# Performance work log

Hardware: AMD Instinct MI355X
Metric: run time of the kernel (lower is better)

Reference implementation:

```python
import jax, jax.numpy as jnp
import numpy as np

B, S, T = 512, 512, 128


def setup_inputs() -> dict:
    key = jax.random.key(0)
    k1, k2, k3, k4, k5 = jax.random.split(key, 5)
    emissions = jax.random.normal(k1, (B, S, T), dtype=jnp.float32)
    tags = jax.random.randint(k2, (B, S), 0, T, dtype=jnp.int32)
    mask = jnp.ones((B, S), dtype=jnp.int32)
    start_transitions = jax.random.uniform(k3, (T,), minval=-0.1, maxval=0.1, dtype=jnp.float32)
    end_transitions = jax.random.uniform(k4, (T,), minval=-0.1, maxval=0.1, dtype=jnp.float32)
    transitions = jax.random.uniform(k5, (T, T), minval=-0.1, maxval=0.1, dtype=jnp.float32)
    return {"emissions": emissions, "tags": tags, "mask": mask,
            "start_transitions": start_transitions,
            "end_transitions": end_transitions,
            "transitions": transitions}


def reference(emissions, tags, mask, start_transitions, end_transitions, transitions):
    b, s, t = emissions.shape
    maskf = mask.astype(emissions.dtype)
    barange = jnp.arange(b)

    # ---- numerator: score of the gold path (vectorized over timesteps) ----
    score = start_transitions[tags[:, 0]] + emissions[barange, 0, tags[:, 0]]
    # transition scores tags[i-1] -> tags[i], shape (B, S-1)
    trans_steps = transitions[tags[:, :-1], tags[:, 1:]]
    # emission score of gold tag at each step, shape (B, S)
    em_steps = jnp.take_along_axis(emissions, tags[:, :, None], axis=2)[:, :, 0]
    score = score + jnp.sum((trans_steps + em_steps[:, 1:]) * maskf[:, 1:], axis=1)
    seq_ends = mask.astype(jnp.int32).sum(axis=1) - 1
    last_tags = tags[barange, seq_ends]
    score = score + end_transitions[last_tags]

    # ---- denominator: log partition via forward recurrence (lax.scan) ----
    init = start_transitions[None, :] + emissions[:, 0, :]  # (B, T)

    def step(scores, inp):
        em_i, m_i = inp  # (B, T), (B,)
        # (B, T_prev, T_next) semiring matmul in log-space
        nxt = jax.nn.logsumexp(
            scores[:, :, None] + transitions[None, :, :] + em_i[:, None, :], axis=1)
        scores = jnp.where(m_i[:, None] > 0, nxt, scores)
        return scores, None

    ems = jnp.moveaxis(emissions[:, 1:, :], 1, 0)  # (S-1, B, T)
    ms = jnp.moveaxis(mask[:, 1:], 1, 0)           # (S-1, B)
    final, _ = jax.lax.scan(step, init, (ems, ms))
    denom = jax.nn.logsumexp(final + end_transitions[None, :], axis=1)  # (B,)

    return jnp.sum(score - denom)
```

## Files before the change

### kernel.cpp

```cpp
#include <hip/hip_runtime.h>
#include <math.h>


#define T 128
#define SLEN 512
#define BATCH 512

typedef float v2f __attribute__((ext_vector_type(2)));

static __device__ __forceinline__ float dpp_xor1(float x) {
    return __int_as_float(__builtin_amdgcn_update_dpp(
        0, __float_as_int(x), 0xB1, 0xF, 0xF, true));
}
static __device__ __forceinline__ float dpp_xor2(float x) {
    return __int_as_float(__builtin_amdgcn_update_dpp(
        0, __float_as_int(x), 0x4E, 0xF, 0xF, true));
}
static __device__ __forceinline__ void lgkm_barrier() {
    asm volatile("s_waitcnt lgkmcnt(0)\n\ts_barrier" ::: "memory");
}
static __device__ __forceinline__ int pslot(int j) {
    return j ^ (((j >> 5) & 3) << 2);
}

__global__ __launch_bounds__(512, 4) void fwd_kernel(
    const float* __restrict__ em, const int* __restrict__ tags,
    const int* __restrict__ mask, const float* __restrict__ startT,
    const float* __restrict__ endT, const float* __restrict__ trans,
    float* __restrict__ ws)
{
    const int tid  = threadIdx.x;
    const int lane = tid & 63;
    const int w    = tid >> 6;
    const int rg   = lane & 3;
    const int cg   = lane >> 2;
    const int b    = blockIdx.x;
    const int mycol = 16 * w + cg;

    const float* emb = em + (size_t)b * SLEN * T;
    const int*   mk  = mask + (size_t)b * SLEN;

    __shared__ __align__(16) float p_lds[2][T];
    __shared__ float reds[8], redn[8];
    __shared__ int   redc[8];

    int rslot[8];
#pragma unroll
    for (int k = 0; k < 8; ++k)
        rslot[k] = (32 * rg + 4 * k) ^ (rg << 2);
    const int wslot = pslot(mycol);

    v2f Elo[8], Ehi[8];
#pragma unroll
    for (int k = 0; k < 8; ++k) {
        const float* tp = trans + (32 * rg + 4 * k) * T + mycol;
        Elo[k] = (v2f){ __expf(tp[0 * T]), __expf(tp[1 * T]) };
        Ehi[k] = (v2f){ __expf(tp[2 * T]), __expf(tp[3 * T]) };
    }

    float pprev = __expf(startT[mycol] + emb[mycol]);
    if (rg == 0) p_lds[1][wslot] = pprev;
    double Ld = 0.0;

    float emv[4], emn[4];
    int   mkv[4], mkn[4];
#pragma unroll
    for (int k = 0; k < 4; ++k) {
        emv[k] = __expf(emb[(1 + k) * T + mycol]);
        mkv[k] = mk[1 + k];
    }
    lgkm_barrier();

    for (int s0 = 1; s0 < SLEN; s0 += 4) {
#pragma unroll
        for (int k = 0; k < 4; ++k) {
            int ss = s0 + 4 + k; ss = (ss < SLEN) ? ss : (SLEN - 1);
            emn[k] = emb[ss * T + mycol];
            mkn[k] = mk[ss];
        }
#pragma unroll
        for (int k = 0; k < 4; ++k) {
            const int s = s0 + k;
            if (s < SLEN) {
                const int cur = (1 + k) & 1;
                const float srefc = fmaxf(p_lds[cur][0], 1e-30f);
                const float cc = __builtin_amdgcn_rcpf(srefc);
                Ld += (double)__logf(srefc);

                v2f pk0[8], pk1[8];
#pragma unroll
                for (int k2 = 0; k2 < 8; ++k2) {
                    const float4 pv = *(const float4*)&p_lds[cur][rslot[k2]];
                    pk0[k2] = (v2f){ pv.x, pv.y };
                    pk1[k2] = (v2f){ pv.z, pv.w };
                }
                v2f accE = pk0[0] * Elo[0];
                v2f accO = pk1[0] * Ehi[0];
#pragma unroll
                for (int k2 = 1; k2 < 8; ++k2) {
                    accE = __builtin_elementwise_fma(pk0[k2], Elo[k2], accE);
                    accO = __builtin_elementwise_fma(pk1[k2], Ehi[k2], accO);
                }
                const v2f accT = accE + accO;
                const float sv = accT.x + accT.y;

                float t = sv + dpp_xor1(sv);
                t = t + dpp_xor2(t);

                const float pn = t * (emv[k] * cc);
                const float pm = pprev * cc;
                pprev = (mkv[k] > 0) ? pn : pm;
                if (rg == 0) p_lds[cur ^ 1][wslot] = pprev;
                lgkm_barrier();
            }
        }
#pragma unroll
        for (int k = 0; k < 4; ++k) { emv[k] = __expf(emn[k]); mkv[k] = mkn[k]; }
    }

    const float eendv = __expf(endT[mycol]);
    float sm = pprev * eendv;
#pragma unroll
    for (int off = 32; off; off >>= 1) sm += __shfl_xor(sm, off);
    if (lane == 0) reds[w] = sm;

    const int* tg = tags + (size_t)b * SLEN;
    float nv = 0.f; int cnt = 0;
    {
        const int s = tid;
        const int mm = mk[s];
        cnt += (mm != 0);
        if (s >= 1 && mm > 0)
            nv += trans[tg[s - 1] * T + tg[s]] + emb[s * T + tg[s]];
    }
#pragma unroll
    for (int off = 32; off; off >>= 1) {
        nv  += __shfl_xor(nv, off);
        cnt += __shfl_xor(cnt, off);
    }
    if (lane == 0) { redn[w] = nv; redc[w] = cnt; }
    __syncthreads();
    if (tid == 0) {
        float ssum = 0.f, nsum = 0.f; int seqlen = 0;
#pragma unroll
        for (int i = 0; i < 8; ++i) {
            ssum += reds[i]; nsum += redn[i]; seqlen += redc[i];
        }
        const float denom = __logf(0.25f * ssum) + (float)Ld;
        const int t0g = tg[0], tl = tg[seqlen - 1];
        ws[b] = (startT[t0g] + emb[t0g] + endT[tl] + nsum) - denom;
    }
}

__global__ __launch_bounds__(256) void reduce_kernel(
    const float* __restrict__ ws, float* __restrict__ out)
{
    const int t = threadIdx.x;
    float local = 0.f;
    for (int i = t; i < BATCH; i += 256) local += ws[i];
    __shared__ float rf[256];
    rf[t] = local;
    __syncthreads();
    for (int off = 128; off > 0; off >>= 1) {
        if (t < off) rf[t] += rf[t + off];
        __syncthreads();
    }
    if (t == 0) out[0] = rf[0];
}

extern "C" void kernel_launch(void* const* d_in, const int* in_sizes, int n_in,
                              void* d_out, int out_size, void* d_ws, size_t ws_size,
                              hipStream_t stream)
{
    const float* emissions = (const float*)d_in[0];
    const int*   tags      = (const int*)d_in[1];
    const int*   mask      = (const int*)d_in[2];
    const float* startT    = (const float*)d_in[3];
    const float* endT      = (const float*)d_in[4];
    const float* trans     = (const float*)d_in[5];
    float* out = (float*)d_out;
    float* ws  = (float*)d_ws;

    fwd_kernel<<<BATCH, 512, 0, stream>>>(emissions, tags, mask, startT, endT, trans, ws);
    reduce_kernel<<<1, 256, 0, stream>>>(ws, out);
}
```

Before: 392.2 us.

## Halve block size with two columns per lane and renormalize once per four steps

Each thread now computes two output columns of the forward recurrence, so a block needs 256 threads instead of 512, and the transition matrix held in registers doubles. The rescaling by the reference probability and the log accumulation now happen only on the first of every four timesteps rather than every step, which removes an LDS read, a reciprocal and a double-precision add from most steps. The per-step DPP reduction is restructured so that the two partial sums per lane pair combine into the right column. Skipping renormalization on three of four steps risks float overflow or underflow over those steps, and the extra registers may lower occupancy.

```diff
diff --git a/kernel.cpp b/kernel.cpp
--- a/kernel.cpp
+++ b/kernel.cpp
@@ -23,7 +23,7 @@
     return j ^ (((j >> 5) & 3) << 2);
 }
 
-__global__ __launch_bounds__(512, 4) void fwd_kernel(
+__global__ __launch_bounds__(256, 2) void fwd_kernel(
     const float* __restrict__ em, const int* __restrict__ tags,
     const int* __restrict__ mask, const float* __restrict__ startT,
     const float* __restrict__ endT, const float* __restrict__ trans,
@@ -35,31 +35,36 @@
     const int rg   = lane & 3;
     const int cg   = lane >> 2;
     const int b    = blockIdx.x;
-    const int mycol = 16 * w + cg;
+    const int rb0  = rg & 1;
+    const int colbase = 32 * w + 2 * cg;
+    const int mycol   = colbase + rb0;
 
     const float* emb = em + (size_t)b * SLEN * T;
     const int*   mk  = mask + (size_t)b * SLEN;
 
     __shared__ __align__(16) float p_lds[2][T];
-    __shared__ float reds[8], redn[8];
-    __shared__ int   redc[8];
+    __shared__ float reds[4], redn[4];
+    __shared__ int   redc[4];
 
     int rslot[8];
 #pragma unroll
-    for (int k = 0; k < 8; ++k)
-        rslot[k] = (32 * rg + 4 * k) ^ (rg << 2);
+    for (int k2 = 0; k2 < 8; ++k2)
+        rslot[k2] = 32 * rg + 4 * (k2 ^ rg);
     const int wslot = pslot(mycol);
 
-    v2f Elo[8], Ehi[8];
-#pragma unroll
-    for (int k = 0; k < 8; ++k) {
-        const float* tp = trans + (32 * rg + 4 * k) * T + mycol;
-        Elo[k] = (v2f){ __expf(tp[0 * T]), __expf(tp[1 * T]) };
-        Ehi[k] = (v2f){ __expf(tp[2 * T]), __expf(tp[3 * T]) };
+    v2f Elo[2][8], Ehi[2][8];
+#pragma unroll
+    for (int k2 = 0; k2 < 8; ++k2) {
+        const float* tp = trans + (32 * rg + 4 * k2) * T + colbase;
+#pragma unroll
+        for (int c = 0; c < 2; ++c) {
+            Elo[c][k2] = (v2f){ __expf(tp[0 * T + c]), __expf(tp[1 * T + c]) };
+            Ehi[c][k2] = (v2f){ __expf(tp[2 * T + c]), __expf(tp[3 * T + c]) };
+        }
     }
 
     float pprev = __expf(startT[mycol] + emb[mycol]);
-    if (rg == 0) p_lds[1][wslot] = pprev;
+    if (rg < 2) p_lds[1][wslot] = pprev;
     double Ld = 0.0;
 
     float emv[4], emn[4];
@@ -83,9 +88,12 @@
             const int s = s0 + k;
             if (s < SLEN) {
                 const int cur = (1 + k) & 1;
-                const float srefc = fmaxf(p_lds[cur][0], 1e-30f);
-                const float cc = __builtin_amdgcn_rcpf(srefc);
-                Ld += (double)__logf(srefc);
+                float cc = 1.0f;
+                if (k == 0) {
+                    const float srefc = fmaxf(p_lds[cur][0], 1e-30f);
+                    cc = __builtin_amdgcn_rcpf(srefc);
+                    Ld += (double)__logf(srefc);
+                }
 
                 v2f pk0[8], pk1[8];
 #pragma unroll
@@ -94,23 +102,30 @@
                     pk0[k2] = (v2f){ pv.x, pv.y };
                     pk1[k2] = (v2f){ pv.z, pv.w };
                 }
-                v2f accE = pk0[0] * Elo[0];
-                v2f accO = pk1[0] * Ehi[0];
+                v2f a0e = pk0[0] * Elo[0][0];
+                v2f a0o = pk1[0] * Ehi[0][0];
+                v2f a1e = pk0[0] * Elo[1][0];
+                v2f a1o = pk1[0] * Ehi[1][0];
 #pragma unroll
                 for (int k2 = 1; k2 < 8; ++k2) {
-                    accE = __builtin_elementwise_fma(pk0[k2], Elo[k2], accE);
-                    accO = __builtin_elementwise_fma(pk1[k2], Ehi[k2], accO);
+                    a0e = __builtin_elementwise_fma(pk0[k2], Elo[0][k2], a0e);
+                    a0o = __builtin_elementwise_fma(pk1[k2], Ehi[0][k2], a0o);
+                    a1e = __builtin_elementwise_fma(pk0[k2], Elo[1][k2], a1e);
+                    a1o = __builtin_elementwise_fma(pk1[k2], Ehi[1][k2], a1o);
                 }
-                const v2f accT = accE + accO;
-                const float sv = accT.x + accT.y;
-
-                float t = sv + dpp_xor1(sv);
-                t = t + dpp_xor2(t);
-
-                const float pn = t * (emv[k] * cc);
-                const float pm = pprev * cc;
+                const v2f s0v = a0e + a0o, s1v = a1e + a1o;
+                const float sv0 = s0v.x + s0v.y;
+                const float sv1 = s1v.x + s1v.y;
+
+                const float v1 = (rb0 ? sv1 : sv0)
+                               + dpp_xor1(rb0 ? sv0 : sv1);
+                const float t  = v1 + dpp_xor2(v1);
+
+                float pn, pm;
+                if (k == 0) { pn = t * (emv[k] * cc); pm = pprev * cc; }
+                else        { pn = t * emv[k];        pm = pprev;      }
                 pprev = (mkv[k] > 0) ? pn : pm;
-                if (rg == 0) p_lds[cur ^ 1][wslot] = pprev;
+                if (rg < 2) p_lds[cur ^ 1][wslot] = pprev;
                 lgkm_barrier();
             }
         }
@@ -126,8 +141,9 @@
 
     const int* tg = tags + (size_t)b * SLEN;
     float nv = 0.f; int cnt = 0;
-    {
-        const int s = tid;
+#pragma unroll
+    for (int rep = 0; rep < 2; ++rep) {
+        const int s = tid + 256 * rep;
         const int mm = mk[s];
         cnt += (mm != 0);
         if (s >= 1 && mm > 0)
@@ -143,10 +159,10 @@
     if (tid == 0) {
         float ssum = 0.f, nsum = 0.f; int seqlen = 0;
 #pragma unroll
-        for (int i = 0; i < 8; ++i) {
+        for (int i = 0; i < 4; ++i) {
             ssum += reds[i]; nsum += redn[i]; seqlen += redc[i];
         }
-        const float denom = __logf(0.25f * ssum) + (float)Ld;
+        const float denom = __logf(0.5f * ssum) + (float)Ld;
         const int t0g = tg[0], tl = tg[seqlen - 1];
         ws[b] = (startT[t0g] + emb[t0g] + endT[tl] + nsum) - denom;
     }
@@ -181,6 +197,6 @@
     float* out = (float*)d_out;
     float* ws  = (float*)d_ws;
 
-    fwd_kernel<<<BATCH, 512, 0, stream>>>(emissions, tags, mask, startT, endT, trans, ws);
+    fwd_kernel<<<BATCH, 256, 0, stream>>>(emissions, tags, mask, startT, endT, trans, ws);
     reduce_kernel<<<1, 256, 0, stream>>>(ws, out);
 }
```

Measured after the change: 336.3 us. -14.3%, faster.
